# Kernel tuning notes

Measured on AMD Instinct MI355X. Metric: run time of the kernel, lower is better.

## Reference

```python
import jax, jax.numpy as jnp
import numpy as np

B, T, D, H1, H2, O = 64, 256, 512, 1024, 1024, 512


def setup_inputs() -> dict:
    key = jax.random.key(0)
    ks = jax.random.split(key, 6)
    s = 0.05  # weight scale for numerical sanity
    return {
        "x": jax.random.normal(ks[0], (B, T, D), dtype=jnp.float32),
        "W1": jax.random.normal(ks[1], (D, 4 * H1), dtype=jnp.float32) * s,
        "U1": jax.random.normal(ks[2], (H1, 4 * H1), dtype=jnp.float32) * s,
        "b1": jnp.zeros((4 * H1,), dtype=jnp.float32),
        "W2": jax.random.normal(ks[3], (H1, 4 * H2), dtype=jnp.float32) * s,
        "U2": jax.random.normal(ks[4], (H2, 4 * H2), dtype=jnp.float32) * s,
        "b2": jnp.zeros((4 * H2,), dtype=jnp.float32),
        "Wd": jax.random.normal(ks[5], (H2, O), dtype=jnp.float32) * s,
        "bd": jnp.zeros((O,), dtype=jnp.float32),
    }


def _lstm_layer(x_seq, W, U, b, units):
    """Run an LSTM layer over x_seq [B,T,Din]; returns full h sequence [B,T,units].

    Keras LSTMCell gate order: i, f, c(g), o; sigmoid recurrent activation, tanh activation.
    """
    # Precompute input projections for all timesteps: [T, B, 4*units]
    xz = (jnp.einsum('btd,dk->tbk', x_seq, W) + b).astype(x_seq.dtype)
    bsz = x_seq.shape[0]
    h0 = jnp.zeros((bsz, units), dtype=x_seq.dtype)
    c0 = jnp.zeros((bsz, units), dtype=x_seq.dtype)

    def step(carry, xz_t):
        h, c = carry
        z = xz_t + h @ U
        zi, zf, zg, zo = jnp.split(z, 4, axis=-1)
        c_new = jax.nn.sigmoid(zf) * c + jax.nn.sigmoid(zi) * jnp.tanh(zg)
        h_new = jax.nn.sigmoid(zo) * jnp.tanh(c_new)
        return (h_new, c_new), h_new

    (_, _), hs = jax.lax.scan(step, (h0, c0), xz)  # hs: [T, B, units]
    return jnp.transpose(hs, (1, 0, 2))


def reference(x, W1, U1, b1, W2, U2, b2, Wd, bd):
    seq1 = _lstm_layer(x, W1, U1, b1, H1)          # [B, T, H1]
    seq2 = _lstm_layer(seq1, W2, U2, b2, H2)       # [B, T, H2]
    h_last = seq2[:, -1, :]                        # final hidden state of layer 2
    return h_last @ Wd + bd
```

## Files before the change

kernel.cpp:

```cpp
#include <hip/hip_runtime.h>


typedef __bf16 bf16x8 __attribute__((ext_vector_type(8)));
typedef float f32x4 __attribute__((ext_vector_type(4)));
typedef unsigned int u32x4 __attribute__((ext_vector_type(4)));
typedef unsigned short u16;

#define LDS_Z_OFF 131584
#define LDS_TOTAL 148992

__device__ __forceinline__ u16 f2bf(float f) {
  unsigned u = __float_as_uint(f);
  unsigned r = (u + 0x7FFFu + ((u >> 16) & 1u)) >> 16;
  return (u16)r;
}

__global__ __launch_bounds__(256) void transpose_to_bf16(
    const float* __restrict__ in, u16* __restrict__ out, int R, int C) {
  __shared__ float tile[32][33];
  int tx = threadIdx.x & 31, ty = threadIdx.x >> 5;
  int c0 = blockIdx.x * 32, r0 = blockIdx.y * 32;
#pragma unroll
  for (int i = 0; i < 4; ++i)
    tile[ty + i * 8][tx] = in[(size_t)(r0 + ty + i * 8) * C + (c0 + tx)];
  __syncthreads();
#pragma unroll
  for (int i = 0; i < 4; ++i)
    out[(size_t)(c0 + ty + i * 8) * R + (r0 + tx)] = f2bf(tile[tx][ty + i * 8]);
}

__global__ __launch_bounds__(256) void convert_to_bf16(
    const float* __restrict__ in, u16* __restrict__ out, int n4) {
  int i = blockIdx.x * 256 + threadIdx.x;
  if (i >= n4) return;
  float4 v = reinterpret_cast<const float4*>(in)[i];
  ushort4 o;
  o.x = f2bf(v.x); o.y = f2bf(v.y); o.z = f2bf(v.z); o.w = f2bf(v.w);
  reinterpret_cast<ushort4*>(out)[i] = o;
}

__global__ void init_bar(unsigned* __restrict__ bar) { bar[threadIdx.x] = 0u; }

__device__ __forceinline__ void store_h_sc1(u16* p, unsigned v) {
  asm volatile("global_store_short %0, %1, off sc1" :: "v"(p), "v"(v) : "memory");
}

template <int I, int C0, int DEPTH, bool SC0, bool SC1>
__device__ __forceinline__ void stg_issue(u32x4 (&ring)[DEPTH],
    const u16* b0, const u16* b1) {
  constexpr int OFF = (I < C0 ? I : I - C0) * 256;
  if constexpr (I < C0) {
    if constexpr (SC0)
      asm volatile("global_load_dwordx4 %0, %1, off offset:%2 sc1"
                   : "=v"(ring[I % DEPTH]) : "v"(b0), "i"(OFF));
    else
      asm volatile("global_load_dwordx4 %0, %1, off offset:%2"
                   : "=v"(ring[I % DEPTH]) : "v"(b0), "i"(OFF));
  } else {
    if constexpr (SC1)
      asm volatile("global_load_dwordx4 %0, %1, off offset:%2 sc1"
                   : "=v"(ring[I % DEPTH]) : "v"(b1), "i"(OFF));
    else
      asm volatile("global_load_dwordx4 %0, %1, off offset:%2"
                   : "=v"(ring[I % DEPTH]) : "v"(b1), "i"(OFF));
  }
}

template <int I, int NPRE, int C0, int DEPTH, bool SC0, bool SC1>
__device__ __forceinline__ void stg_pre(u32x4 (&ring)[DEPTH],
    const u16* b0, const u16* b1) {
  if constexpr (I < NPRE) {
    stg_issue<I, C0, DEPTH, SC0, SC1>(ring, b0, b1);
    stg_pre<I + 1, NPRE, C0, DEPTH, SC0, SC1>(ring, b0, b1);
  }
}

template <int I, int NC, int C0, int DEPTH, bool SC0, bool SC1>
__device__ __forceinline__ void stg_main(u32x4 (&ring)[DEPTH],
    const u16* b0, const u16* b1, u16* lrow) {
  if constexpr (I < NC) {
    constexpr int ISSUED = (I + DEPTH < NC) ? I + DEPTH : NC;
    constexpr int WAIT = ISSUED - I - 1;
    asm volatile("s_waitcnt vmcnt(%1)" : "+v"(ring[I % DEPTH]) : "i"(WAIT));
    *(u32x4*)(lrow + I * 128) = ring[I % DEPTH];
    if constexpr (I + DEPTH < NC)
      stg_issue<I + DEPTH, C0, DEPTH, SC0, SC1>(ring, b0, b1);
    stg_main<I + 1, NC, C0, DEPTH, SC0, SC1>(ring, b0, b1, lrow);
  }
}

template <int NC, int C0, bool SC0, bool SC1>
__device__ __forceinline__ void stage(const u16* b0, const u16* b1, u16* lrow) {
  u32x4 ring[8];
  stg_pre<0, (NC < 8 ? NC : 8), C0, 8, SC0, SC1>(ring, b0, b1);
  stg_main<0, NC, C0, 8, SC0, SC1>(ring, b0, b1, lrow);
}

__device__ __forceinline__ void grid_barrier(unsigned* __restrict__ bar,
                                             int g, unsigned want) {
  asm volatile("s_waitcnt vmcnt(0)" ::: "memory");
  __syncthreads();
  if (threadIdx.x == 0) {
    unsigned old = __hip_atomic_fetch_add(bar + 32 * (1 + g), 1u,
                                          __ATOMIC_RELAXED, __HIP_MEMORY_SCOPE_AGENT);
    if (old == 32u * want - 1u) {
      unsigned r = __hip_atomic_fetch_add(bar, 1u, __ATOMIC_RELAXED,
                                          __HIP_MEMORY_SCOPE_AGENT);
      if (r == 8u * want - 1u) {
#pragma unroll
        for (int i = 0; i < 8; ++i)
          __hip_atomic_store(bar + 32 * (9 + i), want, __ATOMIC_RELAXED,
                             __HIP_MEMORY_SCOPE_AGENT);
      }
    }
    while (__hip_atomic_load(bar + 32 * (9 + g), __ATOMIC_RELAXED,
                             __HIP_MEMORY_SCOPE_AGENT) < want)
      __builtin_amdgcn_s_sleep(1);
  }
  __syncthreads();
}

template <int NC, int C0, bool SC0, bool IS2>
__device__ __forceinline__ void run_layer(
    const u16* __restrict__ xbf, const u16* __restrict__ Wt,
    const u16* __restrict__ Ut, const float* __restrict__ bias,
    u16* __restrict__ h1r, u16* __restrict__ h2r, unsigned* __restrict__ bar,
    int strip, int mhalf, char* smem, int g) {
  constexpr int KE = NC * 128;
  constexpr int P = KE + 8;
  constexpr int NCH = NC * 4;
  constexpr int WCH = C0 * 4;
  constexpr int HALF = NCH / 2;
  u16* Alds = (u16*)smem;
  float* Zlds = (float*)(smem + LDS_Z_OFF);
  const int tid = threadIdx.x;
  const int wave = tid >> 6, lane = tid & 63;
  const int gate = wave & 3, kh = wave >> 2;
  const int quad = lane >> 4, l16 = lane & 15;

  bf16x8 breg[HALF];
  const int col = gate * 1024 + strip * 16 + l16;
  const int kb = kh * HALF;
#pragma unroll
  for (int j = 0; j < HALF; ++j) {
    int ks = kb + j;
    if (ks < WCH)
      breg[j] = *(const bf16x8*)(Wt + (size_t)col * (WCH * 32) + ks * 32 + quad * 8);
    else
      breg[j] = *(const bf16x8*)(Ut + (size_t)col * 1024 + (ks - WCH) * 32 + quad * 8);
  }

  const int eu = tid & 15, em = tid >> 4;
  const float bz0 = bias[strip * 16 + eu];
  const float bz1 = bias[1024 + strip * 16 + eu];
  const float bz2 = bias[2048 + strip * 16 + eu];
  const float bz3 = bias[3072 + strip * 16 + eu];
  float c = 0.f;

  const int sr = tid >> 4, l8 = tid & 15;
  const int sb = mhalf * 32 + sr;
  u16* lrow = Alds + sr * P + l8 * 8;

  const u16* a0p = Alds + l16 * P + quad * 8 + kb * 32;
  const u16* a1p = a0p + 16 * P;

  for (int s = 0; s <= 256; ++s) {
    const int t = IS2 ? (s - 1) : s;
    if (t >= 0 && t < 256) {
      const u16 *b0, *b1;
      if constexpr (IS2) {
        b0 = h1r + (size_t)(t & 1) * 65536 + (size_t)sb * 1024 + l8 * 8;
        b1 = h2r + (size_t)((t - 1) & 1) * 65536 + (size_t)sb * 1024 + l8 * 8;
      } else {
        b0 = xbf + ((size_t)sb * 256 + t) * 512 + l8 * 8;
        b1 = h1r + (size_t)((t - 1) & 1) * 65536 + (size_t)sb * 1024 + l8 * 8;
      }
      if (t > 0) {
        stage<NC, C0, SC0, true>(b0, b1, lrow);
      } else {
        stage<C0, C0, SC0, true>(b0, b0, lrow);
#pragma unroll
        for (int i = C0; i < NC; ++i)
          *(u32x4*)(lrow + i * 128) = (u32x4){0u, 0u, 0u, 0u};
      }
      __syncthreads();

      f32x4 acc0 = {0.f, 0.f, 0.f, 0.f}, acc1 = {0.f, 0.f, 0.f, 0.f};
#pragma unroll
      for (int j = 0; j < HALF; ++j) {
        bf16x8 a0 = *(const bf16x8*)(a0p + j * 32);
        bf16x8 a1 = *(const bf16x8*)(a1p + j * 32);
        acc0 = __builtin_amdgcn_mfma_f32_16x16x32_bf16(a0, breg[j], acc0, 0, 0, 0);
        acc1 = __builtin_amdgcn_mfma_f32_16x16x32_bf16(a1, breg[j], acc1, 0, 0, 0);
      }

      float* zb = Zlds + kh * (32 * 68);
#pragma unroll
      for (int i = 0; i < 4; ++i) {
        zb[(quad * 4 + i) * 68 + gate * 16 + l16] = acc0[i];
        zb[(16 + quad * 4 + i) * 68 + gate * 16 + l16] = acc1[i];
      }
      __syncthreads();

      u16* hring = IS2 ? h2r : h1r;
      u16* hp = hring + (size_t)(t & 1) * 65536 +
                (size_t)(mhalf * 32 + em) * 1024 + strip * 16 + eu;
      {
        float zi = Zlds[em * 68 + eu]      + Zlds[(32 + em) * 68 + eu]      + bz0;
        float zf = Zlds[em * 68 + 16 + eu] + Zlds[(32 + em) * 68 + 16 + eu] + bz1;
        float zg = Zlds[em * 68 + 32 + eu] + Zlds[(32 + em) * 68 + 32 + eu] + bz2;
        float zo = Zlds[em * 68 + 48 + eu] + Zlds[(32 + em) * 68 + 48 + eu] + bz3;
        float ig = 1.f / (1.f + __expf(-zi));
        float fg = 1.f / (1.f + __expf(-zf));
        float gg = 1.f - 2.f / (1.f + __expf(2.f * zg));
        float og = 1.f / (1.f + __expf(-zo));
        c = fg * c + ig * gg;
        float h = og * (1.f - 2.f / (1.f + __expf(2.f * c)));
        store_h_sc1(hp, (unsigned)f2bf(h));
      }
    }
    if (s < 256) grid_barrier(bar, g, (unsigned)(s + 1));
  }
}

__global__ __launch_bounds__(512, 2) void lstm_persistent(
    const u16* __restrict__ xbf,
    const u16* __restrict__ W1t,
    const u16* __restrict__ U1t,
    const float* __restrict__ b1,
    const u16* __restrict__ W2t,
    const u16* __restrict__ U2t,
    const float* __restrict__ b2,
    u16* __restrict__ h1r,
    u16* __restrict__ h2r,
    unsigned* __restrict__ bar) {
  extern __shared__ __align__(16) char smem[];
  const int blk = blockIdx.x;
  const bool is2 = blk >= 128;
  const int lb = is2 ? blk - 128 : blk;
  const int strip = lb >> 1;
  const int mhalf = lb & 1;
  const int g = blk & 7;
  if (!is2)
    run_layer<12, 4, false, false>(xbf, W1t, U1t, b1, h1r, h2r, bar,
                                   strip, mhalf, smem, g);
  else
    run_layer<16, 8, true, true>(xbf, W2t, U2t, b2, h1r, h2r, bar,
                                 strip, mhalf, smem, g);
}

__global__ __launch_bounds__(64) void dense_kernel(
    const u16* __restrict__ h2,
    const u16* __restrict__ Wdt,
    const float* __restrict__ bd,
    float* __restrict__ out) {
  int mt = blockIdx.x >> 5;
  int nt = blockIdx.x & 31;
  int lane = threadIdx.x;
  int quad = lane >> 4, l16 = lane & 15;
  f32x4 acc = {0.f, 0.f, 0.f, 0.f};
  const u16* ap = h2 + (size_t)(mt * 16 + l16) * 1024 + quad * 8;
  const u16* bp = Wdt + (size_t)(nt * 16 + l16) * 1024 + quad * 8;
#pragma unroll
  for (int ks = 0; ks < 32; ++ks) {
    bf16x8 a = *reinterpret_cast<const bf16x8*>(ap + ks * 32);
    bf16x8 b = *reinterpret_cast<const bf16x8*>(bp + ks * 32);
    acc = __builtin_amdgcn_mfma_f32_16x16x32_bf16(a, b, acc, 0, 0, 0);
  }
  int colo = nt * 16 + l16;
  float bias = bd[colo];
#pragma unroll
  for (int i = 0; i < 4; ++i)
    out[(size_t)(mt * 16 + quad * 4 + i) * 512 + colo] = acc[i] + bias;
}

extern "C" void kernel_launch(void* const* d_in, const int* in_sizes, int n_in,
                              void* d_out, int out_size, void* d_ws, size_t ws_size,
                              hipStream_t stream) {
  const float* x  = (const float*)d_in[0];
  const float* W1 = (const float*)d_in[1];
  const float* U1 = (const float*)d_in[2];
  const float* b1 = (const float*)d_in[3];
  const float* W2 = (const float*)d_in[4];
  const float* U2 = (const float*)d_in[5];
  const float* b2 = (const float*)d_in[6];
  const float* Wd = (const float*)d_in[7];
  const float* bd = (const float*)d_in[8];
  float* out = (float*)d_out;

  char* p = (char*)d_ws;
  auto carve = [&](size_t bytes) -> char* {
    char* r = p;
    p += (bytes + 255) & ~(size_t)255;
    return r;
  };
  u16* W1t = (u16*)carve((size_t)4096 * 512 * 2);
  u16* U1t = (u16*)carve((size_t)4096 * 1024 * 2);
  u16* W2t = (u16*)carve((size_t)4096 * 1024 * 2);
  u16* U2t = (u16*)carve((size_t)4096 * 1024 * 2);
  u16* Wdt = (u16*)carve((size_t)512 * 1024 * 2);
  u16* xbf = (u16*)carve((size_t)64 * 256 * 512 * 2);
  u16* h1r = (u16*)carve((size_t)2 * 64 * 1024 * 2);
  u16* h2r = (u16*)carve((size_t)2 * 64 * 1024 * 2);
  unsigned* bar = (unsigned*)carve(1024 * 4);
  (void)ws_size; (void)in_sizes; (void)n_in; (void)out_size;

  transpose_to_bf16<<<dim3(128, 16), 256, 0, stream>>>(W1, W1t, 512, 4096);
  transpose_to_bf16<<<dim3(128, 32), 256, 0, stream>>>(U1, U1t, 1024, 4096);
  transpose_to_bf16<<<dim3(128, 32), 256, 0, stream>>>(W2, W2t, 1024, 4096);
  transpose_to_bf16<<<dim3(128, 32), 256, 0, stream>>>(U2, U2t, 1024, 4096);
  transpose_to_bf16<<<dim3(16, 32), 256, 0, stream>>>(Wd, Wdt, 1024, 512);
  convert_to_bf16<<<8192, 256, 0, stream>>>(x, xbf, 64 * 256 * 512 / 4);
  init_bar<<<1, 1024, 0, stream>>>(bar);

  hipFuncSetAttribute(reinterpret_cast<const void*>(lstm_persistent),
                      hipFuncAttributeMaxDynamicSharedMemorySize, LDS_TOTAL);
  lstm_persistent<<<256, 512, LDS_TOTAL, stream>>>(
      xbf, W1t, U1t, b1, W2t, U2t, b2, h1r, h2r, bar);

  dense_kernel<<<128, 64, 0, stream>>>(h2r + 65536, Wdt, bd, out);
}
```

Before: 1.623 ms.

## Split MFMA work into gate pairs with four-way K split to reuse A fragments

Each of the 8 waves now computes two gate columns over a quarter of the K dimension instead of one gate over half of K. Every A fragment loaded from LDS is reused for two B fragments, halving LDS reads of the activation tile per MFMA. The partial sums are reduced in two phases: waves 0-3 write to LDS, then after a barrier waves 4-7 accumulate into the same slots. This adds an extra __syncthreads per timestep and read-modify-write LDS traffic on the latency-bound recurrent critical path.

```diff
diff --git a/kernel.cpp b/kernel.cpp
--- a/kernel.cpp
+++ b/kernel.cpp
@@ -128,26 +128,25 @@
     int strip, int mhalf, char* smem, int g) {
   constexpr int KE = NC * 128;
   constexpr int P = KE + 8;
-  constexpr int NCH = NC * 4;
   constexpr int WCH = C0 * 4;
-  constexpr int HALF = NCH / 2;
   u16* Alds = (u16*)smem;
   float* Zlds = (float*)(smem + LDS_Z_OFF);
   const int tid = threadIdx.x;
   const int wave = tid >> 6, lane = tid & 63;
-  const int gate = wave & 3, kh = wave >> 2;
+  const int cp = wave & 1, kq = wave >> 1;
   const int quad = lane >> 4, l16 = lane & 15;
 
-  bf16x8 breg[HALF];
-  const int col = gate * 1024 + strip * 16 + l16;
-  const int kb = kh * HALF;
-#pragma unroll
-  for (int j = 0; j < HALF; ++j) {
-    int ks = kb + j;
-    if (ks < WCH)
-      breg[j] = *(const bf16x8*)(Wt + (size_t)col * (WCH * 32) + ks * 32 + quad * 8);
-    else
-      breg[j] = *(const bf16x8*)(Ut + (size_t)col * 1024 + (ks - WCH) * 32 + quad * 8);
+  bf16x8 breg[2][NC];
+#pragma unroll
+  for (int gi = 0; gi < 2; ++gi) {
+    const int col = (2 * cp + gi) * 1024 + strip * 16 + l16;
+#pragma unroll
+    for (int j = 0; j < NC; ++j) {
+      const int ks = kq * NC + j;
+      breg[gi][j] = (ks < WCH)
+        ? *(const bf16x8*)(Wt + (size_t)col * (C0 * 128) + ks * 32 + quad * 8)
+        : *(const bf16x8*)(Ut + (size_t)col * 1024 + (ks - WCH) * 32 + quad * 8);
+    }
   }
 
   const int eu = tid & 15, em = tid >> 4;
@@ -161,8 +160,11 @@
   const int sb = mhalf * 32 + sr;
   u16* lrow = Alds + sr * P + l8 * 8;
 
-  const u16* a0p = Alds + l16 * P + quad * 8 + kb * 32;
+  const u16* a0p = Alds + l16 * P + quad * 8 + kq * (NC * 32);
   const u16* a1p = a0p + 16 * P;
+
+  const int zc0 = cp * 32 + l16, zc1 = zc0 + 16;
+  float* zb = Zlds + (kq & 1) * (32 * 68);
 
   for (int s = 0; s <= 256; ++s) {
     const int t = IS2 ? (s - 1) : s;
@@ -185,20 +187,36 @@
       }
       __syncthreads();
 
-      f32x4 acc0 = {0.f, 0.f, 0.f, 0.f}, acc1 = {0.f, 0.f, 0.f, 0.f};
-#pragma unroll
-      for (int j = 0; j < HALF; ++j) {
+      f32x4 acc00 = {0.f, 0.f, 0.f, 0.f}, acc10 = {0.f, 0.f, 0.f, 0.f};
+      f32x4 acc01 = {0.f, 0.f, 0.f, 0.f}, acc11 = {0.f, 0.f, 0.f, 0.f};
+#pragma unroll
+      for (int j = 0; j < NC; ++j) {
         bf16x8 a0 = *(const bf16x8*)(a0p + j * 32);
         bf16x8 a1 = *(const bf16x8*)(a1p + j * 32);
-        acc0 = __builtin_amdgcn_mfma_f32_16x16x32_bf16(a0, breg[j], acc0, 0, 0, 0);
-        acc1 = __builtin_amdgcn_mfma_f32_16x16x32_bf16(a1, breg[j], acc1, 0, 0, 0);
-      }
-
-      float* zb = Zlds + kh * (32 * 68);
-#pragma unroll
-      for (int i = 0; i < 4; ++i) {
-        zb[(quad * 4 + i) * 68 + gate * 16 + l16] = acc0[i];
-        zb[(16 + quad * 4 + i) * 68 + gate * 16 + l16] = acc1[i];
+        acc00 = __builtin_amdgcn_mfma_f32_16x16x32_bf16(a0, breg[0][j], acc00, 0, 0, 0);
+        acc10 = __builtin_amdgcn_mfma_f32_16x16x32_bf16(a1, breg[0][j], acc10, 0, 0, 0);
+        acc01 = __builtin_amdgcn_mfma_f32_16x16x32_bf16(a0, breg[1][j], acc01, 0, 0, 0);
+        acc11 = __builtin_amdgcn_mfma_f32_16x16x32_bf16(a1, breg[1][j], acc11, 0, 0, 0);
+      }
+
+      if (kq < 2) {
+#pragma unroll
+        for (int i = 0; i < 4; ++i) {
+          zb[(quad * 4 + i) * 68 + zc0] = acc00[i];
+          zb[(16 + quad * 4 + i) * 68 + zc0] = acc10[i];
+          zb[(quad * 4 + i) * 68 + zc1] = acc01[i];
+          zb[(16 + quad * 4 + i) * 68 + zc1] = acc11[i];
+        }
+      }
+      __syncthreads();
+      if (kq >= 2) {
+#pragma unroll
+        for (int i = 0; i < 4; ++i) {
+          zb[(quad * 4 + i) * 68 + zc0] += acc00[i];
+          zb[(16 + quad * 4 + i) * 68 + zc0] += acc10[i];
+          zb[(quad * 4 + i) * 68 + zc1] += acc01[i];
+          zb[(16 + quad * 4 + i) * 68 + zc1] += acc11[i];
+        }
       }
       __syncthreads();
 
```

New measurement: 1.468 ms. 9.6% less time.
